# Optimization experiments

Measured on AMD Instinct MI355X. Metric: run time of the kernel, lower is better.

The kernel has to match this reference:

```python
import jax, jax.numpy as jnp
import numpy as np

N_EMBED = 384
HEAD_SIZE = 64


def setup_inputs() -> dict:
    key = jax.random.key(0)
    ks = jax.random.split(key, 7)
    B, T, C = 512, 256, N_EMBED
    inp = jax.random.normal(ks[0], (B, T, C), dtype=jnp.float32)
    s = 1.0 / np.sqrt(C)
    Wv = jax.random.normal(ks[1], (C, HEAD_SIZE), dtype=jnp.float32) * s
    bv = jax.random.normal(ks[2], (HEAD_SIZE,), dtype=jnp.float32) * 0.02
    Wk = jax.random.normal(ks[3], (C, HEAD_SIZE), dtype=jnp.float32) * s
    bk = jax.random.normal(ks[4], (HEAD_SIZE,), dtype=jnp.float32) * 0.02
    Wq = jax.random.normal(ks[5], (C, HEAD_SIZE), dtype=jnp.float32) * s
    bq = jax.random.normal(ks[6], (HEAD_SIZE,), dtype=jnp.float32) * 0.02
    return {"inp": inp, "Wv": Wv, "bv": bv, "Wk": Wk, "bk": bk, "Wq": Wq, "bq": bq}


def reference(inp, Wv, bv, Wk, bk, Wq, bq):
    B, T, C = inp.shape
    values = inp @ Wv + bv   # [B, T, H]
    keys = inp @ Wk + bk     # [B, T, H]
    queries = inp @ Wq + bq  # [B, T, H]
    # Faithful to source: scores = keys @ queries^T, scaled by C**-0.5 (embed dim)
    scale = C ** (-0.5)
    W = jnp.einsum('bth,bsh->bts', keys, queries) * scale  # [B, T, T]
    causal = jnp.tril(jnp.ones((T, T), dtype=bool))
    W = jnp.where(causal, W, -jnp.inf)
    W = jax.nn.softmax(W, axis=-1)
    out = jnp.einsum('bts,bsh->bth', W, values)  # [B, T, H]
    return out
```

## Files before the change

### kernel.cpp

```cpp
#include <hip/hip_runtime.h>
#include <stdint.h>

typedef short s16x8 __attribute__((ext_vector_type(8)));
typedef float f32x4 __attribute__((ext_vector_type(4)));

#define TT 256
#define CC 384
#define HH 64

__device__ __forceinline__ unsigned short f2bf(float f) {
  union { float f; uint32_t u; } v; v.f = f;
  return (unsigned short)((v.u + 0x7fffu + ((v.u >> 16) & 1u)) >> 16);
}

__global__ __launch_bounds__(256, 1) void attn_head_kernel(
    const float* __restrict__ inp,
    const float* __restrict__ Wv, const float* __restrict__ bv,
    const float* __restrict__ Wk, const float* __restrict__ bk,
    const float* __restrict__ Wq, const float* __restrict__ bq,
    float* __restrict__ out)
{
  __shared__ unsigned short inp_lds[256][40];
  __shared__ unsigned short wt_lds[192][40];
  __shared__ unsigned short K_lds[256 * 64];
  __shared__ unsigned short Q_lds[256 * 64];
  __shared__ unsigned short V_lds[64 * 256];
  __shared__ unsigned short P_lds[4][16][40];

  const int b    = blockIdx.x;
  const int tid  = threadIdx.x;
  const int wave = tid >> 6;
  const int lane = tid & 63;
  const int l15  = lane & 15;
  const int lg   = lane >> 4;

  const float* inp_b = inp + (size_t)b * TT * CC;

  f32x4 acc[4][12];
#pragma unroll
  for (int mf = 0; mf < 4; ++mf)
#pragma unroll
    for (int nf = 0; nf < 12; ++nf)
      acc[mf][nf] = (f32x4){0.f, 0.f, 0.f, 0.f};

  for (int k0 = 0; k0 < CC; k0 += 32) {
    __syncthreads();
#pragma unroll
    for (int it = 0; it < 8; ++it) {
      int idx = tid + it * 256;
      int row = idx >> 3, c4 = idx & 7;
      float4 v = *(const float4*)(inp_b + row * CC + k0 + c4 * 4);
      unsigned short* d = &inp_lds[row][c4 * 4];
      d[0] = f2bf(v.x); d[1] = f2bf(v.y); d[2] = f2bf(v.z); d[3] = f2bf(v.w);
    }
#pragma unroll
    for (int m = 0; m < 3; ++m) {
      const float* W = (m == 0) ? Wk : (m == 1 ? Wq : Wv);
#pragma unroll
      for (int it = 0; it < 2; ++it) {
        int idx = tid + it * 256;
        int kk = idx >> 4, c4 = idx & 15;
        float4 v = *(const float4*)(W + (k0 + kk) * HH + c4 * 4);
        int nb = m * 64 + c4 * 4;
        wt_lds[nb + 0][kk] = f2bf(v.x);
        wt_lds[nb + 1][kk] = f2bf(v.y);
        wt_lds[nb + 2][kk] = f2bf(v.z);
        wt_lds[nb + 3][kk] = f2bf(v.w);
      }
    }
    __syncthreads();
    const int t0base = wave * 64;
    s16x8 bb[12];
#pragma unroll
    for (int nf = 0; nf < 12; ++nf)
      bb[nf] = *(const s16x8*)&wt_lds[nf * 16 + l15][lg * 8];
#pragma unroll
    for (int mf = 0; mf < 4; ++mf) {
      s16x8 a = *(const s16x8*)&inp_lds[t0base + mf * 16 + l15][lg * 8];
#pragma unroll
      for (int nf = 0; nf < 12; ++nf)
        acc[mf][nf] = __builtin_amdgcn_mfma_f32_16x16x32_bf16(a, bb[nf], acc[mf][nf], 0, 0, 0);
    }
  }

  {
    const float scale = 0.05103103630798287f;
    const int t0base = wave * 64;
    char* Kb = (char*)K_lds; char* Qb = (char*)Q_lds; char* Vb = (char*)V_lds;
#pragma unroll
    for (int nf = 0; nf < 12; ++nf) {
      int n = nf * 16 + l15;
      float bias = (n < 64) ? bk[n] : (n < 128 ? bq[n - 64] : bv[n - 128]);
#pragma unroll
      for (int mf = 0; mf < 4; ++mf) {
#pragma unroll
        for (int r = 0; r < 4; ++r) {
          int t = t0base + mf * 16 + lg * 4 + r;
          float x = acc[mf][nf][r] + bias;
          if (n < 64) {
            int off = t * 128 + ((n * 2) ^ ((t & 7) << 4));
            *(unsigned short*)(Kb + off) = f2bf(x * scale);
          } else if (n < 128) {
            int nn = n - 64;
            int off = t * 128 + ((nn * 2) ^ ((t & 7) << 4));
            *(unsigned short*)(Qb + off) = f2bf(x);
          } else {
            int nn = n - 128;
            int off = nn * 512 + ((t * 2) ^ ((nn & 7) << 4));
            *(unsigned short*)(Vb + off) = f2bf(x);
          }
        }
      }
    }
  }
  __syncthreads();

  const char* Kb = (const char*)K_lds;
  const char* Qb = (const char*)Q_lds;
  const char* Vb = (const char*)V_lds;

  for (int ti = 0; ti < 4; ++ti) {
    const int tf = ((ti & 1) ? (7 - wave) : wave) + 8 * (ti >> 1);
    const int t0 = tf * 16;
    float m[4], lsum[4];
    f32x4 O[4];
#pragma unroll
    for (int r = 0; r < 4; ++r) { m[r] = -1e30f; lsum[r] = 0.f; }
#pragma unroll
    for (int nf = 0; nf < 4; ++nf) O[nf] = (f32x4){0.f, 0.f, 0.f, 0.f};

    const int trow = t0 + l15;
    const int swzT = (trow & 7) << 4;

    for (int s0 = 0; s0 < t0 + 16; s0 += 32) {
      f32x4 Sa = {0.f,0.f,0.f,0.f}, Sb = {0.f,0.f,0.f,0.f};
      const int srow = s0 + l15;
      const int swzS = (srow & 7) << 4;
#pragma unroll
      for (int kk = 0; kk < 2; ++kk) {
        int hb = (kk * 32 + lg * 8) * 2;
        s16x8 a  = *(const s16x8*)(Kb + trow * 128 + (hb ^ swzT));
        s16x8 q0 = *(const s16x8*)(Qb + srow * 128 + (hb ^ swzS));
        s16x8 q1 = *(const s16x8*)(Qb + (srow + 16) * 128 + (hb ^ swzS));
        Sa = __builtin_amdgcn_mfma_f32_16x16x32_bf16(a, q0, Sa, 0, 0, 0);
        Sb = __builtin_amdgcn_mfma_f32_16x16x32_bf16(a, q1, Sb, 0, 0, 0);
      }
      float alpha[4], pa[4], pb[4];
#pragma unroll
      for (int r = 0; r < 4; ++r) {
        int t = t0 + lg * 4 + r;
        int sA = s0 + l15;
        float xa = (sA      <= t) ? Sa[r] : -1e30f;
        float xb = (sA + 16 <= t) ? Sb[r] : -1e30f;
        float mx = fmaxf(xa, xb);
#pragma unroll
        for (int d = 1; d < 16; d <<= 1) mx = fmaxf(mx, __shfl_xor(mx, d, 64));
        float mn = fmaxf(m[r], mx);
        alpha[r] = __expf(m[r] - mn);
        m[r] = mn;
        pa[r] = __expf(xa - mn);
        pb[r] = __expf(xb - mn);
        float rs = pa[r] + pb[r];
#pragma unroll
        for (int d = 1; d < 16; d <<= 1) rs += __shfl_xor(rs, d, 64);
        lsum[r] = lsum[r] * alpha[r] + rs;
      }
#pragma unroll
      for (int nf = 0; nf < 4; ++nf)
#pragma unroll
        for (int r = 0; r < 4; ++r) O[nf][r] *= alpha[r];
#pragma unroll
      for (int r = 0; r < 4; ++r) {
        int prow = lg * 4 + r;
        P_lds[wave][prow][l15]      = f2bf(pa[r]);
        P_lds[wave][prow][l15 + 16] = f2bf(pb[r]);
      }
      asm volatile("s_waitcnt lgkmcnt(0)" ::: "memory");
      s16x8 pfrag = *(const s16x8*)&P_lds[wave][l15][lg * 8];
#pragma unroll
      for (int nf = 0; nf < 4; ++nf) {
        int h = nf * 16 + l15;
        int sbyte = (s0 + lg * 8) * 2;
        s16x8 vb = *(const s16x8*)(Vb + h * 512 + (sbyte ^ ((h & 7) << 4)));
        O[nf] = __builtin_amdgcn_mfma_f32_16x16x32_bf16(pfrag, vb, O[nf], 0, 0, 0);
      }
    }
    float* outb = out + ((size_t)b * TT + t0) * HH;
#pragma unroll
    for (int r = 0; r < 4; ++r) {
      float inv = 1.0f / lsum[r];
#pragma unroll
      for (int nf = 0; nf < 4; ++nf)
        outb[(lg * 4 + r) * HH + nf * 16 + l15] = O[nf][r] * inv;
    }
  }
}

extern "C" void kernel_launch(void* const* d_in, const int* in_sizes, int n_in,
                              void* d_out, int out_size, void* d_ws, size_t ws_size,
                              hipStream_t stream) {
  (void)n_in; (void)out_size; (void)d_ws; (void)ws_size;
  const float* inp = (const float*)d_in[0];
  const float* Wv  = (const float*)d_in[1];
  const float* bv  = (const float*)d_in[2];
  const float* Wk  = (const float*)d_in[3];
  const float* bk  = (const float*)d_in[4];
  const float* Wq  = (const float*)d_in[5];
  const float* bq  = (const float*)d_in[6];
  float* out = (float*)d_out;
  const int B = in_sizes[0] / (TT * CC);
  attn_head_kernel<<<B, 256, 0, stream>>>(inp, Wv, bv, Wk, bk, Wq, bq, out);
}
```

Measured before the change: 352.7 us.

## Double block to 8 waves and prefetch next projection chunk into registers

Raises the block from 256 to 512 threads, so each wave handles half as many rows in the QKV projection (32 instead of 64) and two causal query tiles instead of four in attention. It also software-prefetches the next 32-wide chunk of input and weights into registers while the current chunk is converted and stored to LDS, hiding global load latency behind compute. A sched_barrier is added after the P store/wait. Launch bounds change to (512,2), which tightens the per-thread register budget. LDS use (~120KB) likely still allows only one block per CU, and occupancy rises through more waves per block.

```diff
diff --git a/kernel.cpp b/kernel.cpp
--- a/kernel.cpp
+++ b/kernel.cpp
@@ -13,7 +13,7 @@
   return (unsigned short)((v.u + 0x7fffu + ((v.u >> 16) & 1u)) >> 16);
 }
 
-__global__ __launch_bounds__(256, 1) void attn_head_kernel(
+__global__ __launch_bounds__(512, 2) void attn_head_kernel(
     const float* __restrict__ inp,
     const float* __restrict__ Wv, const float* __restrict__ bv,
     const float* __restrict__ Wk, const float* __restrict__ bk,
@@ -25,7 +25,7 @@
   __shared__ unsigned short K_lds[256 * 64];
   __shared__ unsigned short Q_lds[256 * 64];
   __shared__ unsigned short V_lds[64 * 256];
-  __shared__ unsigned short P_lds[4][16][40];
+  __shared__ unsigned short P_lds[8][16][40];
 
   const int b    = blockIdx.x;
   const int tid  = threadIdx.x;
@@ -36,46 +36,66 @@
 
   const float* inp_b = inp + (size_t)b * TT * CC;
 
-  f32x4 acc[4][12];
-#pragma unroll
-  for (int mf = 0; mf < 4; ++mf)
+  f32x4 acc[2][12];
+#pragma unroll
+  for (int mf = 0; mf < 2; ++mf)
 #pragma unroll
     for (int nf = 0; nf < 12; ++nf)
       acc[mf][nf] = (f32x4){0.f, 0.f, 0.f, 0.f};
 
-  for (int k0 = 0; k0 < CC; k0 += 32) {
+  float4 rin[4];
+  float4 rw[3];
+  const int wkk = tid >> 4;
+  const int wc4 = tid & 15;
+
+#pragma unroll
+  for (int it = 0; it < 4; ++it) {
+    int idx = tid + it * 512;
+    int row = idx >> 3, c4 = idx & 7;
+    rin[it] = *(const float4*)(inp_b + row * CC + 0 + c4 * 4);
+  }
+  rw[0] = *(const float4*)(Wk + wkk * HH + wc4 * 4);
+  rw[1] = *(const float4*)(Wq + wkk * HH + wc4 * 4);
+  rw[2] = *(const float4*)(Wv + wkk * HH + wc4 * 4);
+
+  for (int c = 0; c < 12; ++c) {
     __syncthreads();
 #pragma unroll
-    for (int it = 0; it < 8; ++it) {
-      int idx = tid + it * 256;
+    for (int it = 0; it < 4; ++it) {
+      int idx = tid + it * 512;
       int row = idx >> 3, c4 = idx & 7;
-      float4 v = *(const float4*)(inp_b + row * CC + k0 + c4 * 4);
       unsigned short* d = &inp_lds[row][c4 * 4];
-      d[0] = f2bf(v.x); d[1] = f2bf(v.y); d[2] = f2bf(v.z); d[3] = f2bf(v.w);
+      d[0] = f2bf(rin[it].x); d[1] = f2bf(rin[it].y);
+      d[2] = f2bf(rin[it].z); d[3] = f2bf(rin[it].w);
     }
 #pragma unroll
     for (int m = 0; m < 3; ++m) {
-      const float* W = (m == 0) ? Wk : (m == 1 ? Wq : Wv);
-#pragma unroll
-      for (int it = 0; it < 2; ++it) {
-        int idx = tid + it * 256;
-        int kk = idx >> 4, c4 = idx & 15;
-        float4 v = *(const float4*)(W + (k0 + kk) * HH + c4 * 4);
-        int nb = m * 64 + c4 * 4;
-        wt_lds[nb + 0][kk] = f2bf(v.x);
-        wt_lds[nb + 1][kk] = f2bf(v.y);
-        wt_lds[nb + 2][kk] = f2bf(v.z);
-        wt_lds[nb + 3][kk] = f2bf(v.w);
-      }
+      int nb = m * 64 + wc4 * 4;
+      wt_lds[nb + 0][wkk] = f2bf(rw[m].x);
+      wt_lds[nb + 1][wkk] = f2bf(rw[m].y);
+      wt_lds[nb + 2][wkk] = f2bf(rw[m].z);
+      wt_lds[nb + 3][wkk] = f2bf(rw[m].w);
+    }
+    if (c + 1 < 12) {
+      int k0 = (c + 1) * 32;
+#pragma unroll
+      for (int it = 0; it < 4; ++it) {
+        int idx = tid + it * 512;
+        int row = idx >> 3, c4 = idx & 7;
+        rin[it] = *(const float4*)(inp_b + row * CC + k0 + c4 * 4);
+      }
+      rw[0] = *(const float4*)(Wk + (k0 + wkk) * HH + wc4 * 4);
+      rw[1] = *(const float4*)(Wq + (k0 + wkk) * HH + wc4 * 4);
+      rw[2] = *(const float4*)(Wv + (k0 + wkk) * HH + wc4 * 4);
     }
     __syncthreads();
-    const int t0base = wave * 64;
+    const int t0base = wave * 32;
     s16x8 bb[12];
 #pragma unroll
     for (int nf = 0; nf < 12; ++nf)
       bb[nf] = *(const s16x8*)&wt_lds[nf * 16 + l15][lg * 8];
 #pragma unroll
-    for (int mf = 0; mf < 4; ++mf) {
+    for (int mf = 0; mf < 2; ++mf) {
       s16x8 a = *(const s16x8*)&inp_lds[t0base + mf * 16 + l15][lg * 8];
 #pragma unroll
       for (int nf = 0; nf < 12; ++nf)
@@ -85,14 +105,14 @@
 
   {
     const float scale = 0.05103103630798287f;
-    const int t0base = wave * 64;
+    const int t0base = wave * 32;
     char* Kb = (char*)K_lds; char* Qb = (char*)Q_lds; char* Vb = (char*)V_lds;
 #pragma unroll
     for (int nf = 0; nf < 12; ++nf) {
       int n = nf * 16 + l15;
       float bias = (n < 64) ? bk[n] : (n < 128 ? bq[n - 64] : bv[n - 128]);
 #pragma unroll
-      for (int mf = 0; mf < 4; ++mf) {
+      for (int mf = 0; mf < 2; ++mf) {
 #pragma unroll
         for (int r = 0; r < 4; ++r) {
           int t = t0base + mf * 16 + lg * 4 + r;
@@ -119,8 +139,8 @@
   const char* Qb = (const char*)Q_lds;
   const char* Vb = (const char*)V_lds;
 
-  for (int ti = 0; ti < 4; ++ti) {
-    const int tf = ((ti & 1) ? (7 - wave) : wave) + 8 * (ti >> 1);
+  for (int ti = 0; ti < 2; ++ti) {
+    const int tf = ti ? (15 - wave) : wave;
     const int t0 = tf * 16;
     float m[4], lsum[4];
     f32x4 O[4];
@@ -176,6 +196,7 @@
         P_lds[wave][prow][l15 + 16] = f2bf(pb[r]);
       }
       asm volatile("s_waitcnt lgkmcnt(0)" ::: "memory");
+      __builtin_amdgcn_sched_barrier(0);
       s16x8 pfrag = *(const s16x8*)&P_lds[wave][l15][lg * 8];
 #pragma unroll
       for (int nf = 0; nf < 4; ++nf) {
@@ -209,5 +230,5 @@
   const float* bq  = (const float*)d_in[6];
   float* out = (float*)d_out;
   const int B = in_sizes[0] / (TT * CC);
-  attn_head_kernel<<<B, 256, 0, stream>>>(inp, Wv, bv, Wk, bk, Wq, bq, out);
+  attn_head_kernel<<<B, 512, 0, stream>>>(inp, Wv, bv, Wk, bk, Wq, bq, out);
 }
```

Measured after the change: 324.3 us. 8.1% less time.
